# Kernel optimization log

Hardware: AMD Instinct MI355X
Metric: run time of the kernel (lower is better)

The kernel has to match this reference:

```python
import jax, jax.numpy as jnp
import numpy as np

NUM_HEADS = 12
ROPE_THETA = 10000.0


def setup_inputs() -> dict:
    key = jax.random.key(0)
    ks = jax.random.split(key, 7)
    B, H, W, C = 4, 32, 32, 768
    hd = C // NUM_HEADS
    x = jax.random.normal(ks[0], (B, H, W, C), jnp.float32)
    qkv_w = jax.random.normal(ks[1], (3 * C, C), jnp.float32) * 0.02
    qkv_b = jax.random.normal(ks[2], (3 * C,), jnp.float32) * 0.02
    proj_w = jax.random.normal(ks[3], (C, C), jnp.float32) * 0.02
    proj_b = jax.random.normal(ks[4], (C,), jnp.float32) * 0.02
    rel_pos_h = jax.random.normal(ks[5], (2 * H - 1, hd), jnp.float32) * 0.02
    rel_pos_w = jax.random.normal(ks[6], (2 * W - 1, hd), jnp.float32) * 0.02
    return {"x": x, "qkv_w": qkv_w, "qkv_b": qkv_b, "proj_w": proj_w,
            "proj_b": proj_b, "rel_pos_h": rel_pos_h, "rel_pos_w": rel_pos_w}


def _axial_cis(hd, H, W, theta):
    # compute_axial_cis: frequencies over head_dim//4 bands per axis
    freqs = 1.0 / (theta ** (jnp.arange(0, hd, 4, dtype=jnp.float32)[: hd // 4] / hd))
    t = jnp.arange(H * W, dtype=jnp.float32)
    t_x = t % H          # end_x = input_size[0]
    t_y = jnp.floor(t / H)
    ang = jnp.concatenate([jnp.outer(t_x, freqs), jnp.outer(t_y, freqs)], axis=-1)  # (L, hd//2)
    return jax.lax.complex(jnp.cos(ang), jnp.sin(ang))


def _rope(x, cis):
    # x: (B, nh, L, hd); pairs of channels -> complex, rotate, back to real
    B, nh, L, hd = x.shape
    xr = x.reshape(B, nh, L, hd // 2, 2)
    xc = jax.lax.complex(xr[..., 0], xr[..., 1]) * cis[None, None]
    return jnp.stack([jnp.real(xc), jnp.imag(xc)], axis=-1).reshape(B, nh, L, hd)


def reference(x, qkv_w, qkv_b, proj_w, proj_b, rel_pos_h, rel_pos_w):
    B, H, W, C = x.shape
    nh = NUM_HEADS
    hd = C // nh
    L = H * W
    # fused QKV projection
    qkv = x.reshape(B, L, C) @ qkv_w.T + qkv_b              # (B, L, 3C)
    qkv = qkv.reshape(B, L, 3, nh, hd).transpose(2, 0, 3, 1, 4)
    q, k, v = qkv[0], qkv[1], qkv[2]                        # (B, nh, L, hd)
    # 2D axial RoPE on q, k
    cis = _axial_cis(hd, H, W, ROPE_THETA)
    q = _rope(q, cis)
    k = _rope(k, cis)
    # decomposed relative position bias (math of concat_rel_pos + SDPA w/ rescale)
    coords = jnp.arange(H)[:, None] - jnp.arange(W)[None, :] + (H - 1)  # (H, W), H == W
    Rh = rel_pos_h[coords]                                  # (q_h, k_h, hd)
    Rw = rel_pos_w[coords]                                  # (q_w, k_w, hd)
    rq = q.reshape(B, nh, H, W, hd)
    rel_h = jnp.einsum('bnhwc,hkc->bnhwk', rq, Rh)          # (B, nh, H, W, k_h)
    rel_w = jnp.einsum('bnhwc,wkc->bnhwk', rq, Rw)          # (B, nh, H, W, k_w)
    bias = (rel_h[..., :, None] + rel_w[..., None, :]).reshape(B, nh, L, L)
    scale = 1.0 / jnp.sqrt(jnp.float32(hd))
    scores = jnp.einsum('bnqc,bnkc->bnqk', q, k) * scale + bias
    attn = jax.nn.softmax(scores, axis=-1)
    out = jnp.einsum('bnqk,bnkc->bnqc', attn, v)            # (B, nh, L, hd)
    out = out.transpose(0, 2, 1, 3).reshape(B, H, W, C)
    return out @ proj_w.T + proj_b
```

## Files before the change

kernel.cpp:

```cpp
#include <hip/hip_runtime.h>
#include <hip/hip_bf16.h>
#include <stdint.h>

typedef __hip_bfloat16 bf16;
typedef __attribute__((ext_vector_type(8))) short bf16x8;
typedef __attribute__((ext_vector_type(4))) float f32x4;

#define MFMA16(a, b, c) __builtin_amdgcn_mfma_f32_16x16x32_bf16(a, b, c, 0, 0, 0)

__device__ __forceinline__ void gl_lds16(const void* g, void* l) {
  __builtin_amdgcn_global_load_lds(
      (const __attribute__((address_space(1))) uint32_t*)g,
      (__attribute__((address_space(3))) uint32_t*)l, 16, 0, 0);
}

struct alignas(8) bf16x4s { bf16 a, b, c, d; };

__device__ __forceinline__ void cast4(const float* __restrict__ src,
                                      bf16* __restrict__ dst, int i) {
  float4 v = ((const float4*)src)[i];
  bf16x4s o{__float2bfloat16(v.x), __float2bfloat16(v.y),
            __float2bfloat16(v.z), __float2bfloat16(v.w)};
  ((bf16x4s*)dst)[i] = o;
}

__global__ void k_prep(const float* __restrict__ x, const float* __restrict__ qkvw,
                       const float* __restrict__ projw, bf16* __restrict__ xb,
                       bf16* __restrict__ wqkvb, bf16* __restrict__ wprojb,
                       float* __restrict__ cosT, float* __restrict__ sinT) {
  const int bid = blockIdx.x, tid = threadIdx.x;
  if (bid < 3072) {
    cast4(x, xb, bid * 256 + tid);
  } else if (bid < 4800) {
    cast4(qkvw, wqkvb, (bid - 3072) * 256 + tid);
  } else if (bid < 5376) {
    cast4(projw, wprojb, (bid - 4800) * 256 + tid);
  } else {
    const int i = (bid - 5376) * 256 + tid;
    const int pos = i >> 5, p = i & 31;
    const int j = p & 15;
    const float t = (p < 16) ? (float)(pos & 31) : (float)(pos >> 5);
    const float f = powf(10000.0f, -(float)j / 16.0f);
    float sv, cv;
    sincosf(t * f, &sv, &cv);
    cosT[i] = cv;
    sinT[i] = sv;
  }
}

template <int BM, int BN>
__device__ __forceinline__ void gemm_loop(const bf16* __restrict__ A,
                                          const bf16* __restrict__ Bt,
                                          int m0, int n0, bf16* ldsA, bf16* ldsB,
                                          f32x4* acc) {
  constexpr int FM = BM / 32, FN = BN / 32;
  constexpr int AL = BM / 64, BL = BN / 64;
  constexpr int ABYTES = BM * 64, BBYTES = BN * 64;
  const int tid = threadIdx.x;
  const int lane = tid & 63, w = tid >> 6;
  const int wm = w >> 1, wn = w & 1;
  const int lr = lane & 15, lg = lane >> 4;

  auto stage = [&](int kt, int buf) {
#pragma unroll
    for (int c = 0; c < AL; ++c) {
      const int o = c * 4096 + w * 1024 + lane * 16;
      gl_lds16((const char*)A + ((size_t)(m0 + (o >> 6)) * 768 + kt) * 2 + (o & 63),
               (char*)ldsA + buf * ABYTES + c * 4096 + w * 1024);
    }
#pragma unroll
    for (int c = 0; c < BL; ++c) {
      const int o = c * 4096 + w * 1024 + lane * 16;
      gl_lds16((const char*)Bt + ((size_t)(n0 + (o >> 6)) * 768 + kt) * 2 + (o & 63),
               (char*)ldsB + buf * BBYTES + c * 4096 + w * 1024);
    }
  };

  stage(0, 0);
  int cur = 0;
  for (int ki = 0; ki < 24; ++ki) {
    if (ki + 1 < 24) {
      stage((ki + 1) * 32, cur ^ 1);
      if constexpr (AL + BL == 2) asm volatile("s_waitcnt vmcnt(2)" ::: "memory");
      else if constexpr (AL + BL == 3) asm volatile("s_waitcnt vmcnt(3)" ::: "memory");
      else asm volatile("s_waitcnt vmcnt(4)" ::: "memory");
    } else {
      asm volatile("s_waitcnt vmcnt(0)" ::: "memory");
    }
    __builtin_amdgcn_s_barrier();
    const char* baseA = (const char*)ldsA + cur * ABYTES;
    const char* baseB = (const char*)ldsB + cur * BBYTES;
    bf16x8 af[FM], bf_[FN];
#pragma unroll
    for (int f = 0; f < FM; ++f)
      af[f] = *(const bf16x8*)(baseA + (wm * (BM / 2) + f * 16 + lr) * 64 + lg * 16);
#pragma unroll
    for (int f = 0; f < FN; ++f)
      bf_[f] = *(const bf16x8*)(baseB + (wn * (BN / 2) + f * 16 + lr) * 64 + lg * 16);
    __builtin_amdgcn_s_setprio(1);
#pragma unroll
    for (int fm = 0; fm < FM; ++fm)
#pragma unroll
      for (int fn = 0; fn < FN; ++fn)
        acc[fm * FN + fn] = MFMA16(af[fm], bf_[fn], acc[fm * FN + fn]);
    __builtin_amdgcn_s_setprio(0);
    asm volatile("s_waitcnt lgkmcnt(0)" ::: "memory");
    __builtin_amdgcn_s_barrier();
    cur ^= 1;
  }
}

__global__ __launch_bounds__(256, 6) void k_qkv(
    const bf16* __restrict__ xb, const bf16* __restrict__ wb, const float* __restrict__ qkvb,
    const float* __restrict__ cosT, const float* __restrict__ sinT,
    bf16* __restrict__ Qb, bf16* __restrict__ Kb, bf16* __restrict__ VbT) {
  __shared__ __align__(16) bf16 ldsA[2][64 * 32];
  __shared__ __align__(16) bf16 ldsB[2][128 * 32];
  const int m0 = (blockIdx.x & 63) * 64, n0 = (blockIdx.x >> 6) * 128;
  f32x4 acc[2 * 4] = {};
  gemm_loop<64, 128>(xb, wb, m0, n0, &ldsA[0][0], &ldsB[0][0], acc);
  const int lane = threadIdx.x & 63, w = threadIdx.x >> 6;
  const int wm = w >> 1, wn = w & 1, lr = lane & 15, lg = lane >> 4;
#pragma unroll
  for (int fm = 0; fm < 2; ++fm) {
#pragma unroll
    for (int fn = 0; fn < 4; ++fn) {
      const int n = n0 + wn * 64 + fn * 16 + lr;
      const int sect = n / 768;
      const int cn = n - sect * 768;
      const int head = cn >> 6, d = cn & 63;
      const float bias = qkvb[n];
      const int p = d >> 1;
#pragma unroll
      for (int r = 0; r < 4; ++r) {
        const int m = m0 + wm * 32 + fm * 16 + lg * 4 + r;
        const int bb = m >> 10, pos = m & 1023;
        float val = acc[fm * 4 + fn][r] + bias;
        const float partner = __shfl_xor(val, 1);
        if (sect < 2) {
          const float cv = cosT[pos * 32 + p], sv = sinT[pos * 32 + p];
          val = (d & 1) ? (val * cv + partner * sv) : (val * cv - partner * sv);
        }
        const bf16 o = __float2bfloat16(val);
        const size_t base = (size_t)(bb * 12 + head) * 65536;
        if (sect == 0)      Qb[base + (size_t)pos * 64 + d] = o;
        else if (sect == 1) Kb[base + (size_t)pos * 64 + d] = o;
        else                VbT[base + (size_t)d * 1024 + pos] = o;
      }
    }
  }
}

__global__ __launch_bounds__(256) void k_relbias(
    const bf16* __restrict__ Qb, const float* __restrict__ relph,
    const float* __restrict__ relpw, float* __restrict__ relh,
    float* __restrict__ relw) {
  const int bid = blockIdx.x;
  const int bn = bid >> 4;
  const int rem = bid & 15;
  const bool isW = (rem >> 3) != 0;
  const int w = threadIdx.x >> 6;
  const int rc = (rem & 7) * 4 + w;
  const int lane = threadIdx.x & 63;
  const int lr = lane & 15, lg = lane >> 4;
  const float* __restrict__ relp = isW ? relpw : relph;

  bf16x8 af[2][2];
#pragma unroll
  for (int mb = 0; mb < 2; ++mb) {
    const int m = mb * 16 + lr;
    const int l = isW ? (m * 32 + rc) : (rc * 32 + m);
    const bf16* ap = Qb + (size_t)bn * 65536 + (size_t)l * 64 + lg * 8;
#pragma unroll
    for (int ks = 0; ks < 2; ++ks) af[mb][ks] = *(const bf16x8*)(ap + ks * 32);
  }
  bf16x8 bfr[2][2];
#pragma unroll
  for (int nb = 0; nb < 2; ++nb) {
    const int n = nb * 16 + lr;
    const float* bp = relp + (size_t)(31 + rc - n) * 64 + lg * 8;
#pragma unroll
    for (int ks = 0; ks < 2; ++ks) {
      const float4 f0 = *(const float4*)(bp + ks * 32);
      const float4 f1 = *(const float4*)(bp + ks * 32 + 4);
      bf16x8 t;
      ((bf16*)&t)[0] = __float2bfloat16(f0.x);
      ((bf16*)&t)[1] = __float2bfloat16(f0.y);
      ((bf16*)&t)[2] = __float2bfloat16(f0.z);
      ((bf16*)&t)[3] = __float2bfloat16(f0.w);
      ((bf16*)&t)[4] = __float2bfloat16(f1.x);
      ((bf16*)&t)[5] = __float2bfloat16(f1.y);
      ((bf16*)&t)[6] = __float2bfloat16(f1.z);
      ((bf16*)&t)[7] = __float2bfloat16(f1.w);
      bfr[nb][ks] = t;
    }
  }
  f32x4 acc[2][2] = {};
#pragma unroll
  for (int ks = 0; ks < 2; ++ks)
#pragma unroll
    for (int mb = 0; mb < 2; ++mb)
#pragma unroll
      for (int nb = 0; nb < 2; ++nb)
        acc[mb][nb] = MFMA16(af[mb][ks], bfr[nb][ks], acc[mb][nb]);
  float* __restrict__ dst = isW ? relw : relh;
#pragma unroll
  for (int mb = 0; mb < 2; ++mb)
#pragma unroll
    for (int nb = 0; nb < 2; ++nb)
#pragma unroll
      for (int r = 0; r < 4; ++r) {
        const int mo = mb * 16 + lg * 4 + r;
        const int n = nb * 16 + lr;
        const int l = isW ? (mo * 32 + rc) : (rc * 32 + mo);
        dst[(size_t)bn * 32768 + (size_t)l * 32 + n] = acc[mb][nb][r];
      }
}

__global__ __launch_bounds__(256, 3) void k_attn(
    const bf16* __restrict__ Qb, const bf16* __restrict__ Kb, const bf16* __restrict__ VbT,
    const float* __restrict__ relh, const float* __restrict__ relw, bf16* __restrict__ attno) {
  __shared__ __align__(16) bf16 Kt[2][64 * 64];
  __shared__ __align__(16) bf16 Vt[2][64 * 64];
  __shared__ __align__(16) float bH[64 * 33];
  __shared__ __align__(16) bf16 Pl[4][16 * 64];
  const int blk0 = blockIdx.x;
  const int blk = (blk0 & 7) * 96 + (blk0 >> 3);
  const int bn = blk >> 4, qt = blk & 15;
  const int b = bn / 12, head = bn - b * 12;
  const int tid = threadIdx.x;
  const int lane = tid & 63, w = tid >> 6;
  const int lr = lane & 15, lg = lane >> 4;
  const size_t qkvbase = (size_t)bn * 65536;

  auto stageKV = [&](int kt, int buf) {
#pragma unroll
    for (int c = 0; c < 2; ++c) {
      const int off = c * 4096 + w * 1024 + lane * 16;
      const int row = off >> 7;
      const int loff = off ^ ((row & 7) << 4);
      gl_lds16((const char*)Kb + (qkvbase + (size_t)kt * 4096) * 2 + loff,
               (char*)Kt + buf * 8192 + c * 4096 + w * 1024);
      gl_lds16((const char*)VbT + (qkvbase + (size_t)row * 1024 + (size_t)kt * 64) * 2 + (loff & 127),
               (char*)Vt + buf * 8192 + c * 4096 + w * 1024);
    }
  };

  stageKV(0, 0);
  {
    const int r = tid >> 2, q8 = (tid & 3) * 8;
    const float* src = relh + (size_t)bn * 32768 + (size_t)(qt * 64 + r) * 32 + q8;
#pragma unroll
    for (int jj = 0; jj < 8; ++jj) bH[r * 33 + q8 + jj] = src[jj];
  }
  const int qrow_g = qt * 64 + w * 16 + lr;
  float bw[2][4];
  {
    const float* rw = relw + (size_t)bn * 32768 + (size_t)qrow_g * 32;
#pragma unroll
    for (int s1 = 0; s1 < 2; ++s1)
#pragma unroll
      for (int r = 0; r < 4; ++r) bw[s1][r] = rw[s1 * 16 + lg * 4 + r];
  }
  bf16x8 qf[2];
  {
    const char* qp = (const char*)(Qb + qkvbase + (size_t)qrow_g * 64);
    qf[0] = *(const bf16x8*)(qp + lg * 16);
    qf[1] = *(const bf16x8*)(qp + 64 + lg * 16);
  }
  f32x4 oacc[4] = {};
  float psum = 0.0f;
  asm volatile("s_waitcnt lgkmcnt(0)" ::: "memory");
  __builtin_amdgcn_s_barrier();
  int cur = 0;

  for (int kt = 0; kt < 16; ++kt) {
    if (kt + 1 < 16) {
      stageKV(kt + 1, cur ^ 1);
      asm volatile("s_waitcnt vmcnt(4)" ::: "memory");
    } else {
      asm volatile("s_waitcnt vmcnt(0)" ::: "memory");
    }
    __builtin_amdgcn_s_barrier();
    const char* Ktc = (const char*)Kt + cur * 8192;
    const char* Vtc = (const char*)Vt + cur * 8192;
    f32x4 sa[4];
    const int sw = (lr & 7) << 4;
    __builtin_amdgcn_s_setprio(1);
#pragma unroll
    for (int s = 0; s < 4; ++s) {
      const int krow = s * 16 + lr;
      bf16x8 k0 = *(const bf16x8*)(Ktc + ((krow * 128 + lg * 16) ^ sw));
      bf16x8 k1 = *(const bf16x8*)(Ktc + ((krow * 128 + 64 + lg * 16) ^ sw));
      f32x4 z = {};
      z = MFMA16(k0, qf[0], z);
      z = MFMA16(k1, qf[1], z);
      sa[s] = z;
    }
    __builtin_amdgcn_s_setprio(0);
    const float bh0 = bH[(w * 16 + lr) * 33 + 2 * kt];
    const float bh1 = bH[(w * 16 + lr) * 33 + 2 * kt + 1];
    short4 pk[4];
#pragma unroll
    for (int s = 0; s < 4; ++s) {
      const float bh = (s < 2) ? bh0 : bh1;
#pragma unroll
      for (int r = 0; r < 4; ++r) {
        const float p = __expf(sa[s][r] * 0.125f + bh + bw[s & 1][r]);
        psum += p;
        ((bf16*)&pk[s])[r] = __float2bfloat16(p);
      }
    }
#pragma unroll
    for (int s = 0; s < 4; ++s) {
      int byteoff = (lr * 128 + s * 32 + lg * 8) ^ sw;
      *(short4*)((char*)Pl[w] + byteoff) = pk[s];
    }
    asm volatile("s_waitcnt lgkmcnt(0)" ::: "memory");
    __builtin_amdgcn_s_setprio(1);
#pragma unroll
    for (int kh = 0; kh < 2; ++kh) {
      const int abyte = (lr * 128 + kh * 64 + lg * 16) ^ sw;
      const bf16x8 pa = *(const bf16x8*)((const char*)Pl[w] + abyte);
#pragma unroll
      for (int dblk = 0; dblk < 4; ++dblk) {
        const int vrow = dblk * 16 + lr;
        const bf16x8 vb = *(const bf16x8*)(Vtc + ((vrow * 128 + kh * 64 + lg * 16) ^ sw));
        oacc[dblk] = MFMA16(pa, vb, oacc[dblk]);
      }
    }
    __builtin_amdgcn_s_setprio(0);
    asm volatile("s_waitcnt lgkmcnt(0)" ::: "memory");
    __builtin_amdgcn_s_barrier();
    cur ^= 1;
  }
  psum += __shfl_xor(psum, 16);
  psum += __shfl_xor(psum, 32);
#pragma unroll
  for (int r = 0; r < 4; ++r) {
    const float lsum = __shfl(psum, lg * 4 + r);
    const float inv = 1.0f / lsum;
    const int qg = qt * 64 + w * 16 + lg * 4 + r;
#pragma unroll
    for (int dblk = 0; dblk < 4; ++dblk) {
      attno[((size_t)b * 1024 + qg) * 768 + head * 64 + dblk * 16 + lr] =
          __float2bfloat16(oacc[dblk][r] * inv);
    }
  }
}

__global__ __launch_bounds__(256, 4) void k_proj(
    const bf16* __restrict__ attno, const bf16* __restrict__ pwb,
    const float* __restrict__ projb, float* __restrict__ out) {
  __shared__ __align__(16) bf16 ldsA[2][64 * 32];
  __shared__ __align__(16) bf16 ldsB[2][64 * 32];
  const int m0 = (blockIdx.x & 63) * 64, n0 = (blockIdx.x >> 6) * 64;
  f32x4 acc[2 * 2] = {};
  gemm_loop<64, 64>(attno, pwb, m0, n0, &ldsA[0][0], &ldsB[0][0], acc);
  const int lane = threadIdx.x & 63, w = threadIdx.x >> 6;
  const int wm = w >> 1, wn = w & 1, lr = lane & 15, lg = lane >> 4;
#pragma unroll
  for (int fm = 0; fm < 2; ++fm) {
#pragma unroll
    for (int fn = 0; fn < 2; ++fn) {
      const int n = n0 + wn * 32 + fn * 16 + lr;
      const float bias = projb[n];
#pragma unroll
      for (int r = 0; r < 4; ++r) {
        const int m = m0 + wm * 32 + fm * 16 + lg * 4 + r;
        out[(size_t)m * 768 + n] = acc[fm * 2 + fn][r] + bias;
      }
    }
  }
}

extern "C" void kernel_launch(void* const* d_in, const int* in_sizes, int n_in,
                              void* d_out, int out_size, void* d_ws, size_t ws_size,
                              hipStream_t stream) {
  const float* x     = (const float*)d_in[0];
  const float* qkvw  = (const float*)d_in[1];
  const float* qkvb  = (const float*)d_in[2];
  const float* projw = (const float*)d_in[3];
  const float* projb = (const float*)d_in[4];
  const float* relph = (const float*)d_in[5];
  const float* relpw = (const float*)d_in[6];
  float* out = (float*)d_out;
  char* ws = (char*)d_ws;

  bf16*  xb     = (bf16*)(ws);
  bf16*  wqkvb  = (bf16*)(ws + 6291456);
  bf16*  wprojb = (bf16*)(ws + 9830400);
  float* cosT   = (float*)(ws + 11010048);
  float* sinT   = (float*)(ws + 11141120);
  bf16*  Qb     = (bf16*)(ws + 11272192);
  bf16*  Kb     = (bf16*)(ws + 17563648);
  bf16*  VbT    = (bf16*)(ws + 23855104);
  float* relh   = (float*)(ws + 30146560);
  float* relw   = (float*)(ws + 36438016);
  bf16*  attno  = (bf16*)(ws + 42729472);

  k_prep<<<5504, 256, 0, stream>>>(x, qkvw, projw, xb, wqkvb, wprojb, cosT, sinT);
  k_qkv<<<1152, 256, 0, stream>>>(xb, wqkvb, qkvb, cosT, sinT, Qb, Kb, VbT);
  k_relbias<<<768, 256, 0, stream>>>(Qb, relph, relpw, relh, relw);
  k_attn<<<768, 256, 0, stream>>>(Qb, Kb, VbT, relh, relw, attno);
  k_proj<<<768, 256, 0, stream>>>(attno, wprojb, projb, out);
}
```

Baseline: 93.59 us.

## Swap MFMA operands so accumulators hold contiguous columns for vectorized epilogue stores

Swaps the A/B operands of the MFMA calls in the shared GEMM loop and in the attention PV product, so each lane's four accumulator values run along the output column dimension. The QKV, attention and projection epilogues then use float4 bias loads and short4/float4 vector stores in place of scalar strided stores. RoPE pairs now sit within a lane, which removes the cross-lane shuffle. A redundant pre-loop barrier in the attention kernel is also dropped. The transposed V stores stay scalar, and the change relies on the swapped layout being consistent in every epilogue.

```diff
diff --git a/kernel.cpp b/kernel.cpp
--- a/kernel.cpp
+++ b/kernel.cpp
@@ -102,7 +102,7 @@
     for (int fm = 0; fm < FM; ++fm)
 #pragma unroll
       for (int fn = 0; fn < FN; ++fn)
-        acc[fm * FN + fn] = MFMA16(af[fm], bf_[fn], acc[fm * FN + fn]);
+        acc[fm * FN + fn] = MFMA16(bf_[fn], af[fm], acc[fm * FN + fn]);
     __builtin_amdgcn_s_setprio(0);
     asm volatile("s_waitcnt lgkmcnt(0)" ::: "memory");
     __builtin_amdgcn_s_barrier();
@@ -123,29 +123,35 @@
   const int wm = w >> 1, wn = w & 1, lr = lane & 15, lg = lane >> 4;
 #pragma unroll
   for (int fm = 0; fm < 2; ++fm) {
+    const int m = m0 + wm * 32 + fm * 16 + lr;
+    const int bb = m >> 10, pos = m & 1023;
 #pragma unroll
     for (int fn = 0; fn < 4; ++fn) {
-      const int n = n0 + wn * 64 + fn * 16 + lr;
-      const int sect = n / 768;
-      const int cn = n - sect * 768;
-      const int head = cn >> 6, d = cn & 63;
-      const float bias = qkvb[n];
-      const int p = d >> 1;
-#pragma unroll
-      for (int r = 0; r < 4; ++r) {
-        const int m = m0 + wm * 32 + fm * 16 + lg * 4 + r;
-        const int bb = m >> 10, pos = m & 1023;
-        float val = acc[fm * 4 + fn][r] + bias;
-        const float partner = __shfl_xor(val, 1);
-        if (sect < 2) {
-          const float cv = cosT[pos * 32 + p], sv = sinT[pos * 32 + p];
-          val = (d & 1) ? (val * cv + partner * sv) : (val * cv - partner * sv);
-        }
-        const bf16 o = __float2bfloat16(val);
-        const size_t base = (size_t)(bb * 12 + head) * 65536;
-        if (sect == 0)      Qb[base + (size_t)pos * 64 + d] = o;
-        else if (sect == 1) Kb[base + (size_t)pos * 64 + d] = o;
-        else                VbT[base + (size_t)d * 1024 + pos] = o;
+      const int nb = n0 + wn * 64 + fn * 16 + lg * 4;
+      const int sect = nb / 768;
+      const int cnb = nb - sect * 768;
+      const int head = cnb >> 6, db = cnb & 63;
+      const float4 b4 = *(const float4*)(qkvb + nb);
+      const f32x4 a = acc[fm * 4 + fn];
+      const float v0 = a[0] + b4.x, v1 = a[1] + b4.y;
+      const float v2 = a[2] + b4.z, v3 = a[3] + b4.w;
+      const size_t base = (size_t)(bb * 12 + head) * 65536;
+      if (sect < 2) {
+        const int p0 = db >> 1;
+        const float c0 = cosT[pos * 32 + p0], s0 = sinT[pos * 32 + p0];
+        const float c1 = cosT[pos * 32 + p0 + 1], s1 = sinT[pos * 32 + p0 + 1];
+        short4 st;
+        ((bf16*)&st)[0] = __float2bfloat16(v0 * c0 - v1 * s0);
+        ((bf16*)&st)[1] = __float2bfloat16(v1 * c0 + v0 * s0);
+        ((bf16*)&st)[2] = __float2bfloat16(v2 * c1 - v3 * s1);
+        ((bf16*)&st)[3] = __float2bfloat16(v3 * c1 + v2 * s1);
+        bf16* dst = (sect == 0 ? Qb : Kb) + base + (size_t)pos * 64 + db;
+        *(short4*)dst = st;
+      } else {
+        VbT[base + (size_t)(db + 0) * 1024 + pos] = __float2bfloat16(v0);
+        VbT[base + (size_t)(db + 1) * 1024 + pos] = __float2bfloat16(v1);
+        VbT[base + (size_t)(db + 2) * 1024 + pos] = __float2bfloat16(v2);
+        VbT[base + (size_t)(db + 3) * 1024 + pos] = __float2bfloat16(v3);
       }
     }
   }
@@ -270,8 +276,6 @@
   }
   f32x4 oacc[4] = {};
   float psum = 0.0f;
-  asm volatile("s_waitcnt lgkmcnt(0)" ::: "memory");
-  __builtin_amdgcn_s_barrier();
   int cur = 0;
 
   for (int kt = 0; kt < 16; ++kt) {
@@ -326,7 +330,7 @@
       for (int dblk = 0; dblk < 4; ++dblk) {
         const int vrow = dblk * 16 + lr;
         const bf16x8 vb = *(const bf16x8*)(Vtc + ((vrow * 128 + kh * 64 + lg * 16) ^ sw));
-        oacc[dblk] = MFMA16(pa, vb, oacc[dblk]);
+        oacc[dblk] = MFMA16(vb, pa, oacc[dblk]);
       }
     }
     __builtin_amdgcn_s_setprio(0);
@@ -336,16 +340,14 @@
   }
   psum += __shfl_xor(psum, 16);
   psum += __shfl_xor(psum, 32);
-#pragma unroll
-  for (int r = 0; r < 4; ++r) {
-    const float lsum = __shfl(psum, lg * 4 + r);
-    const float inv = 1.0f / lsum;
-    const int qg = qt * 64 + w * 16 + lg * 4 + r;
-#pragma unroll
-    for (int dblk = 0; dblk < 4; ++dblk) {
-      attno[((size_t)b * 1024 + qg) * 768 + head * 64 + dblk * 16 + lr] =
-          __float2bfloat16(oacc[dblk][r] * inv);
-    }
+  const float inv = 1.0f / psum;
+#pragma unroll
+  for (int dblk = 0; dblk < 4; ++dblk) {
+    short4 st;
+#pragma unroll
+    for (int r = 0; r < 4; ++r)
+      ((bf16*)&st)[r] = __float2bfloat16(oacc[dblk][r] * inv);
+    *(short4*)(attno + ((size_t)b * 1024 + qrow_g) * 768 + head * 64 + dblk * 16 + lg * 4) = st;
   }
 }
 
@@ -361,15 +363,14 @@
   const int wm = w >> 1, wn = w & 1, lr = lane & 15, lg = lane >> 4;
 #pragma unroll
   for (int fm = 0; fm < 2; ++fm) {
+    const int m = m0 + wm * 32 + fm * 16 + lr;
 #pragma unroll
     for (int fn = 0; fn < 2; ++fn) {
-      const int n = n0 + wn * 32 + fn * 16 + lr;
-      const float bias = projb[n];
-#pragma unroll
-      for (int r = 0; r < 4; ++r) {
-        const int m = m0 + wm * 32 + fm * 16 + lg * 4 + r;
-        out[(size_t)m * 768 + n] = acc[fm * 2 + fn][r] + bias;
-      }
+      const int nb = n0 + wn * 32 + fn * 16 + lg * 4;
+      const float4 b4 = *(const float4*)(projb + nb);
+      const f32x4 a = acc[fm * 2 + fn];
+      float4 o{a[0] + b4.x, a[1] + b4.y, a[2] + b4.z, a[3] + b4.w};
+      *(float4*)(out + (size_t)m * 768 + nb) = o;
     }
   }
 }
```

New measurement: 91.52 us (median of 3 runs). -2.2%, faster.
